# Kernel optimization log

Measured on AMD Instinct MI355X. Metric: run time of the kernel, lower is better.

## Reference

```python
import jax, jax.numpy as jnp
import numpy as np

V = 50000      # vocab_size
E = 512        # embed_size
H = 512        # hidden_size
B = 128        # batch
S = 256        # encoder seq len
MAX_OOVS = 12


def setup_inputs() -> dict:
    key = jax.random.key(0)
    ks = jax.random.split(key, 18)
    s = 0.05
    embed_table = jax.random.normal(ks[4], (V, E), jnp.float32) * s
    embed_table = embed_table.at[0].set(0.0)  # padding_idx=0
    return {
        'input_idx':   jax.random.randint(ks[0], (B,), 0, V),
        'encoded':     jax.random.normal(ks[1], (B, S, H), jnp.float32),
        'encoded_idx': jax.random.randint(ks[2], (B, S), 0, V),
        'prev_state':  jax.random.normal(ks[3], (B, H), jnp.float32),
        'weighted':    jnp.zeros((B, 1, H), jnp.float32),
        'embed_table': embed_table,
        'Ws_w':    jax.random.normal(ks[5], (H, H), jnp.float32) * s,
        'Ws_b':    jnp.zeros((H,), jnp.float32),
        'gru_Wih': jax.random.normal(ks[6], (3 * H, E + H), jnp.float32) * s,
        'gru_Whh': jax.random.normal(ks[7], (3 * H, H), jnp.float32) * s,
        'gru_bih': jnp.zeros((3 * H,), jnp.float32),
        'gru_bhh': jnp.zeros((3 * H,), jnp.float32),
        'attn_W':  jax.random.normal(ks[8], (H, 2 * H), jnp.float32) * s,
        'attn_b':  jnp.zeros((H,), jnp.float32),
        'attn_v':  jax.random.normal(ks[9], (H,), jnp.float32) * s,
        'Wo_w':    jax.random.normal(ks[10], (V, 2 * H), jnp.float32) * s,
        'Wo_b':    jnp.zeros((V,), jnp.float32),
        'Wc_w':    jax.random.normal(ks[11], (2 * H, H), jnp.float32) * s,
        'Wc_b':    jnp.zeros((2 * H,), jnp.float32),
    }


def copy_decoder_fwd(input_idx, encoded, encoded_idx, prev_state, weighted,
                     embed_table, Ws_w, Ws_b, gru_Wih, gru_Whh, gru_bih, gru_bhh,
                     attn_W, attn_b, attn_v, Wo_w, Wo_b, Wc_w, Wc_b):
    b, seq, hidden = encoded.shape
    vocab = Wo_w.shape[0]
    dt = encoded.dtype

    # order == 0 branch: project prev_state, zero the weighted context
    prev = prev_state @ Ws_w.T + Ws_b                      # (b, h)
    wtd = jnp.zeros((b, hidden), dt)                       # (b, h)

    # GRU single step (PyTorch gate layout: r, z, n)
    x = jnp.concatenate([embed_table[input_idx], wtd], axis=1)  # (b, e+h)
    gi = x @ gru_Wih.T + gru_bih                           # (b, 3h)
    gh = prev @ gru_Whh.T + gru_bhh                        # (b, 3h)
    i_r, i_z, i_n = jnp.split(gi, 3, axis=1)
    h_r, h_z, h_n = jnp.split(gh, 3, axis=1)
    r = jax.nn.sigmoid(i_r + h_r)
    z = jax.nn.sigmoid(i_z + h_z)
    n = jnp.tanh(i_n + r * h_n)
    state = (1.0 - z) * n + z * prev                       # (b, h), == rnn_output

    # 'concat' attention: softmax_seq(v . tanh(W[h; enc] + b))
    h_exp = jnp.broadcast_to(state[:, None, :], (b, seq, hidden))
    energy = jnp.tanh(jnp.concatenate([h_exp, encoded], axis=-1) @ attn_W.T + attn_b)
    attn_w = jax.nn.softmax(energy @ attn_v, axis=1)       # (b, seq)
    context = jnp.einsum('bs,bsh->bh', attn_w, encoded)    # (b, h)

    # generation scores
    score_g = jnp.concatenate([state, context], axis=1) @ Wo_w.T + Wo_b  # (b, V)

    # copy scores
    sc = jnp.tanh(encoded @ Wc_w.T + Wc_b)                 # (b, seq, 2h)
    score_c = jnp.einsum('bsk,bk->bs', sc, jnp.concatenate([state, context], axis=1))
    score_c = score_c + jnp.where(encoded_idx == 0, -1000.0, 0.0).astype(dt)

    # joint softmax over vocab + seq
    probs = jax.nn.softmax(jnp.concatenate([score_g, score_c], axis=1), axis=1)
    prob_g = probs[:, :vocab]                              # (b, V)
    prob_c = probs[:, vocab:]                              # (b, seq)
    prob_c_given = prob_c / jnp.sum(prob_c)                # global-scalar normalization (faithful)

    # pad generation probs with small oov mass
    vext = vocab + MAX_OOVS
    prob_g_ext = jnp.concatenate(
        [prob_g, jnp.full((b, MAX_OOVS), 1e-4, dt)], axis=1)  # (b, V+oov)

    # copy -> vocab scatter-add (replaces dense one-hot + bmm)
    batch_ids = jnp.broadcast_to(jnp.arange(b)[:, None], (b, seq))
    prob_c_to_g = jnp.zeros((b, vext), dt).at[batch_ids, encoded_idx].add(prob_c)

    out = (prob_g_ext + prob_c_to_g)[:, None, :]           # (b, 1, V+oov)

    # positions in source equal to the current input token
    ind = (encoded_idx == input_idx[:, None]).astype(dt)   # (b, seq)
    ssum = ind.sum(axis=1, keepdims=True)
    ind = jnp.where(ssum > 1.0, ind / ssum, ind)
    attn2 = prob_c_given * ind                             # (b, seq)
    weighted_new = jnp.einsum('bs,bsh->bh', attn2, encoded)[:, None, :]  # (b, 1, h)

    return out, state, weighted_new


def reference(input_idx, encoded, encoded_idx, prev_state, weighted,
              embed_table, Ws_w, Ws_b, gru_Wih, gru_Whh, gru_bih, gru_bhh,
              attn_W, attn_b, attn_v, Wo_w, Wo_b, Wc_w, Wc_b):
    return copy_decoder_fwd(input_idx, encoded, encoded_idx, prev_state, weighted,
                            embed_table, Ws_w, Ws_b, gru_Wih, gru_Whh, gru_bih, gru_bhh,
                            attn_W, attn_b, attn_v, Wo_w, Wo_b, Wc_w, Wc_b)
```

## Files before the change

### kernel.cpp

```cpp
#include <hip/hip_runtime.h>
#include <hip/hip_bf16.h>
#include <math.h>

#define BB 128
#define SS 256
#define HH 512
#define VV 50000
#define VEXT 50012
#define NBLK 782
#define PST 784

typedef __bf16 bf16x8 __attribute__((ext_vector_type(8)));
typedef float f32x4 __attribute__((ext_vector_type(4)));

__device__ __forceinline__ float fast_tanh(float x) {
  float e = __expf(2.0f * x);
  return 1.0f - 2.0f / (e + 1.0f);
}
__device__ __forceinline__ float fast_sigmoid(float x) {
  return 1.0f / (1.0f + __expf(-x));
}
__device__ __forceinline__ bf16x8 cvt8(const float* p) {
  float4 a = *(const float4*)p;
  float4 b = *(const float4*)(p + 4);
  bf16x8 r;
  r[0] = (__bf16)a.x; r[1] = (__bf16)a.y; r[2] = (__bf16)a.z; r[3] = (__bf16)a.w;
  r[4] = (__bf16)b.x; r[5] = (__bf16)b.y; r[6] = (__bf16)b.z; r[7] = (__bf16)b.w;
  return r;
}

__global__ void k_pack_all(const float* __restrict__ Wc_w, const float* __restrict__ attn_W,
                           const float* __restrict__ enc,
                           __hip_bfloat16* __restrict__ wc_bf,
                           __hip_bfloat16* __restrict__ wa_bf,
                           __hip_bfloat16* __restrict__ epk,
                           float* __restrict__ pc_total) {
  int i = blockIdx.x * 256 + threadIdx.x;
  if (blockIdx.x == 0 && threadIdx.x == 0) pc_total[0] = 0.f;
  if (i < 65536) {
    int l = i & 63, ks = (i >> 6) & 15, tile = i >> 10;
    int m = l & 15, q = l >> 4;
    const float* p = Wc_w + (size_t)(tile * 16 + m) * 512 + ks * 32 + q * 8;
    *(bf16x8*)(wc_bf + (size_t)i * 8) = cvt8(p);
  } else if (i < 98304) {
    int j = i - 65536;
    int l = j & 63, ks = (j >> 6) & 15, tile = j >> 10;
    int m = l & 15, q = l >> 4;
    const float* p = attn_W + (size_t)(tile * 16 + m) * 1024 + 512 + ks * 32 + q * 8;
    *(bf16x8*)(wa_bf + (size_t)j * 8) = cvt8(p);
  } else if (i < 98304 + 2097152) {
    int j = i - 98304;
    int l = j & 63, ks = (j >> 6) & 15, st = (j >> 10) & 15, b = j >> 14;
    int m = l & 15, q = l >> 4;
    const float* p = enc + ((size_t)b * SS + st * 16 + m) * HH + ks * 32 + q * 8;
    *(bf16x8*)(epk + (size_t)j * 8) = cvt8(p);
  }
}

__global__ void k_pack_y(const float* __restrict__ y, __hip_bfloat16* __restrict__ ypk) {
  int i = blockIdx.x * 256 + threadIdx.x;
  int l = i & 63, ks = (i >> 6) & 31, tile = i >> 11;
  int m = l & 15, q = l >> 4;
  const float* p = y + (size_t)(tile * 16 + m) * 1024 + ks * 32 + q * 8;
  *(bf16x8*)(ypk + (size_t)i * 8) = cvt8(p);
}

template <int LDB, bool GATHER>
__global__ __launch_bounds__(256, 2) void k_gemm_bt(
    const float* __restrict__ A, const float* __restrict__ B,
    const float* __restrict__ bias, float* __restrict__ C, int ldc,
    const int* __restrict__ gidx) {
  __shared__ __hip_bfloat16 ylds[128 * 72];
  const int t = threadIdx.x;
  const int l = t & 63, w = t >> 6;
  const int m = l & 15, q = l >> 4;
  const int n = blockIdx.x * 64 + w * 16 + m;
  const float* wrow = B + (size_t)n * LDB;
  f32x4 acc[8];
#pragma unroll
  for (int mt = 0; mt < 8; ++mt) acc[mt] = (f32x4){0.f, 0.f, 0.f, 0.f};

  for (int kt = 0; kt < 512; kt += 64) {
    __syncthreads();
#pragma unroll
    for (int i = 0; i < 8; ++i) {
      int f = t + i * 256;
      int row = f >> 4, c4 = f & 15;
      const float* arow;
      if (GATHER)
        arow = A + (size_t)gidx[row] * 512;
      else
        arow = A + (size_t)row * 512;
      float4 v = *(const float4*)(arow + kt + c4 * 4);
      __hip_bfloat16* d = ylds + row * 72 + c4 * 4;
      d[0] = __float2bfloat16(v.x); d[1] = __float2bfloat16(v.y);
      d[2] = __float2bfloat16(v.z); d[3] = __float2bfloat16(v.w);
    }
    __syncthreads();
#pragma unroll
    for (int ksl = 0; ksl < 2; ++ksl) {
      bf16x8 bfr = cvt8(wrow + kt + ksl * 32 + q * 8);
#pragma unroll
      for (int mt = 0; mt < 8; ++mt) {
        bf16x8 af = *(const bf16x8*)(ylds + (mt * 16 + m) * 72 + ksl * 32 + q * 8);
        acc[mt] = __builtin_amdgcn_mfma_f32_16x16x32_bf16(af, bfr, acc[mt], 0, 0, 0);
      }
    }
  }
  float bv = bias[n];
#pragma unroll
  for (int mt = 0; mt < 8; ++mt) {
#pragma unroll
    for (int r = 0; r < 4; ++r) {
      int rowm = mt * 16 + q * 4 + r;
      C[(size_t)rowm * ldc + n] = acc[mt][r] + bv;
    }
  }
}

__global__ void k_gates(const float* __restrict__ gi, const float* __restrict__ gh,
                        const float* __restrict__ prevv, float* __restrict__ state,
                        float* __restrict__ state_out) {
  int i = blockIdx.x * 256 + threadIdx.x;
  int b = i >> 9, h = i & 511;
  const float* gib = gi + (size_t)b * 1536;
  const float* ghb = gh + (size_t)b * 1536;
  float ir = gib[h], iz = gib[512 + h], inn = gib[1024 + h];
  float hr = ghb[h], hz = ghb[512 + h], hn = ghb[1024 + h];
  float r = fast_sigmoid(ir + hr);
  float z = fast_sigmoid(iz + hz);
  float n = fast_tanh(inn + r * hn);
  float st = (1.f - z) * n + z * prevv[i];
  state[i] = st;
  state_out[i] = st;
}

template <int NTOT, int MODE>
__global__ __launch_bounds__(256, 3) void k_fused(
    const __hip_bfloat16* __restrict__ epack, const __hip_bfloat16* __restrict__ wpk,
    const float* __restrict__ biasA, const float* __restrict__ multA,
    const int* __restrict__ enc_idx, float* __restrict__ out) {
  const int b = blockIdx.x, s0 = blockIdx.y * 32, t = threadIdx.x;
  const int l = t & 63, w = t >> 6;
  const int wm = w & 1, wn = w >> 1;
  const int m = l & 15, q = l >> 4;
  __shared__ float bias_l[NTOT];
  __shared__ float mult_l[NTOT];
  __shared__ float red[2][32];
  const float* bias_base = (MODE == 0) ? biasA + (size_t)b * HH : biasA;
  const float* mult_base = (MODE == 0) ? multA : multA + (size_t)b * 1024;
  for (int i = t; i < NTOT; i += 256) {
    bias_l[i] = bias_base[i];
    mult_l[i] = mult_base[i];
  }
  const int st = blockIdx.y * 2 + wm;
  const __hip_bfloat16* ep = epack + ((size_t)(b * 16 + st) * 16) * 512 + (size_t)l * 8;
  bf16x8 afr[16];
#pragma unroll
  for (int ks = 0; ks < 16; ++ks) afr[ks] = *(const bf16x8*)(ep + ks * 512);
  __syncthreads();

  float part[4] = {0.f, 0.f, 0.f, 0.f};
  for (int nb = 0; nb < NTOT; nb += 32) {
    const __hip_bfloat16* wp = wpk + ((size_t)((nb >> 4) + wn) * 16) * 512 + (size_t)l * 8;
    bf16x8 bfr[16];
#pragma unroll
    for (int ks = 0; ks < 16; ++ks) bfr[ks] = *(const bf16x8*)(wp + ks * 512);
    f32x4 a0 = {0.f, 0.f, 0.f, 0.f}, a1 = a0, a2 = a0, a3 = a0;
#pragma unroll
    for (int j = 0; j < 4; ++j) {
      a0 = __builtin_amdgcn_mfma_f32_16x16x32_bf16(afr[j], bfr[j], a0, 0, 0, 0);
      a1 = __builtin_amdgcn_mfma_f32_16x16x32_bf16(afr[4 + j], bfr[4 + j], a1, 0, 0, 0);
      a2 = __builtin_amdgcn_mfma_f32_16x16x32_bf16(afr[8 + j], bfr[8 + j], a2, 0, 0, 0);
      a3 = __builtin_amdgcn_mfma_f32_16x16x32_bf16(afr[12 + j], bfr[12 + j], a3, 0, 0, 0);
    }
    f32x4 acc = (a0 + a1) + (a2 + a3);
    const int n = nb + wn * 16 + m;
    float bias = bias_l[n];
    float mul = mult_l[n];
#pragma unroll
    for (int r = 0; r < 4; ++r) part[r] += fast_tanh(acc[r] + bias) * mul;
  }
#pragma unroll
  for (int r = 0; r < 4; ++r) {
    part[r] += __shfl_xor(part[r], 1, 64);
    part[r] += __shfl_xor(part[r], 2, 64);
    part[r] += __shfl_xor(part[r], 4, 64);
    part[r] += __shfl_xor(part[r], 8, 64);
  }
  if (m == 0) {
#pragma unroll
    for (int r = 0; r < 4; ++r) red[wn][wm * 16 + q * 4 + r] = part[r];
  }
  __syncthreads();
  if (t < 32) {
    float v = red[0][t] + red[1][t];
    int s = s0 + t;
    if (MODE == 1 && enc_idx[b * SS + s] == 0) v -= 1000.0f;
    out[b * SS + s] = v;
  }
}

__global__ __launch_bounds__(256, 4) void k_score_g2(
    const __hip_bfloat16* __restrict__ ypk, const float* __restrict__ Wo_w,
    const float* __restrict__ Wo_b, float* __restrict__ sg,
    float* __restrict__ ppmax, float* __restrict__ ppsum) {
  const int t = threadIdx.x;
  const int l = t & 63, w = t >> 6;
  const int m = l & 15, q = l >> 4;
  const int blk = blockIdx.x;
  const int n = blk * 64 + w * 16 + m;
  const int n_ld = (n < VV) ? n : (VV - 1);
  const float* wrow = Wo_w + (size_t)n_ld * 1024;
  f32x4 acc[8];
#pragma unroll
  for (int mt = 0; mt < 8; ++mt) acc[mt] = (f32x4){0.f, 0.f, 0.f, 0.f};

  for (int ks = 0; ks < 32; ++ks) {
    bf16x8 bfr = cvt8(wrow + ks * 32 + q * 8);
#pragma unroll
    for (int mt = 0; mt < 8; ++mt) {
      bf16x8 af = *(const bf16x8*)(ypk + (((size_t)mt * 32 + ks) * 64 + l) * 8);
      acc[mt] = __builtin_amdgcn_mfma_f32_16x16x32_bf16(af, bfr, acc[mt], 0, 0, 0);
    }
  }

  float bv = (n < VV) ? Wo_b[n] : 0.f;
#pragma unroll
  for (int mt = 0; mt < 8; ++mt) {
#pragma unroll
    for (int r = 0; r < 4; ++r) {
      float v = acc[mt][r] + bv;
      if (n < VV)
        sg[(size_t)(mt * 16 + q * 4 + r) * VV + n] = v;
      else
        v = -1e30f;
      acc[mt][r] = v;
    }
  }

  __shared__ float redA[4][128];
  __shared__ float MS[128];
#pragma unroll
  for (int mt = 0; mt < 8; ++mt) {
#pragma unroll
    for (int r = 0; r < 4; ++r) {
      float mx = acc[mt][r];
      mx = fmaxf(mx, __shfl_xor(mx, 1, 64));
      mx = fmaxf(mx, __shfl_xor(mx, 2, 64));
      mx = fmaxf(mx, __shfl_xor(mx, 4, 64));
      mx = fmaxf(mx, __shfl_xor(mx, 8, 64));
      if (m == 0) redA[w][mt * 16 + q * 4 + r] = mx;
    }
  }
  __syncthreads();
  if (t < 128)
    MS[t] = fmaxf(fmaxf(redA[0][t], redA[1][t]), fmaxf(redA[2][t], redA[3][t]));
  __syncthreads();
#pragma unroll
  for (int mt = 0; mt < 8; ++mt) {
#pragma unroll
    for (int r = 0; r < 4; ++r) {
      float s = __expf(acc[mt][r] - MS[mt * 16 + q * 4 + r]);
      s += __shfl_xor(s, 1, 64);
      s += __shfl_xor(s, 2, 64);
      s += __shfl_xor(s, 4, 64);
      s += __shfl_xor(s, 8, 64);
      if (m == 0) redA[w][mt * 16 + q * 4 + r] = s;
    }
  }
  __syncthreads();
  if (t < 128) {
    ppmax[(size_t)t * PST + blk] = MS[t];
    ppsum[(size_t)t * PST + blk] = redA[0][t] + redA[1][t] + redA[2][t] + redA[3][t];
  }
}

__global__ void k_rowstat_merge(const float* __restrict__ ppmax, const float* __restrict__ ppsum,
                                const float* __restrict__ sc,
                                float* __restrict__ rmax, float* __restrict__ rsum) {
  const int row = blockIdx.x, t = threadIdx.x;
  __shared__ float rb[8];
  __shared__ float MS[1];
  float mrow = sc[row * SS + t];
  for (int i = t; i < NBLK; i += 256) mrow = fmaxf(mrow, ppmax[(size_t)row * PST + i]);
  for (int off = 32; off > 0; off >>= 1) mrow = fmaxf(mrow, __shfl_xor(mrow, off, 64));
  if ((t & 63) == 0) rb[t >> 6] = mrow;
  __syncthreads();
  if (t == 0) MS[0] = fmaxf(fmaxf(rb[0], rb[1]), fmaxf(rb[2], rb[3]));
  __syncthreads();
  float M = MS[0];
  float s = __expf(sc[row * SS + t] - M);
  for (int i = t; i < NBLK; i += 256)
    s += ppsum[(size_t)row * PST + i] * __expf(ppmax[(size_t)row * PST + i] - M);
  for (int off = 32; off > 0; off >>= 1) s += __shfl_xor(s, off, 64);
  if ((t & 63) == 0) rb[4 + (t >> 6)] = s;
  __syncthreads();
  if (t == 0) {
    rmax[row] = M;
    rsum[row] = rb[4] + rb[5] + rb[6] + rb[7];
  }
}

__global__ void k_attn_softmax(const float* __restrict__ score, float* __restrict__ aw) {
  const int b = blockIdx.x, t = threadIdx.x;
  __shared__ float rbuf[8];
  __shared__ float MS[2];
  float x = score[b * SS + t];
  float m = x;
  for (int off = 32; off > 0; off >>= 1) m = fmaxf(m, __shfl_xor(m, off, 64));
  if ((t & 63) == 0) rbuf[t >> 6] = m;
  __syncthreads();
  if (t == 0) MS[0] = fmaxf(fmaxf(rbuf[0], rbuf[1]), fmaxf(rbuf[2], rbuf[3]));
  __syncthreads();
  float e = __expf(x - MS[0]);
  float s = e;
  for (int off = 32; off > 0; off >>= 1) s += __shfl_xor(s, off, 64);
  if ((t & 63) == 0) rbuf[4 + (t >> 6)] = s;
  __syncthreads();
  if (t == 0) MS[1] = rbuf[4] + rbuf[5] + rbuf[6] + rbuf[7];
  __syncthreads();
  aw[b * SS + t] = e / MS[1];
}

__global__ void k_context(const float* __restrict__ aw, const float* __restrict__ enc,
                          const float* __restrict__ state, float* __restrict__ y) {
  const int b = blockIdx.x, hc = blockIdx.y, t = threadIdx.x;
  __shared__ float aws[SS];
  aws[t] = aw[b * SS + t];
  aws[t + 128] = aw[b * SS + t + 128];
  __syncthreads();
  int h = hc * 128 + t;
  float acc = 0.f;
  for (int s = 0; s < SS; ++s) acc += aws[s] * enc[((size_t)b * SS + s) * HH + h];
  y[(size_t)b * 1024 + HH + h] = acc;
  y[(size_t)b * 1024 + h] = state[b * HH + h];
}

__global__ void k_write_probg(const float* __restrict__ sg,
                              const float* __restrict__ rmax,
                              const float* __restrict__ rsum,
                              float* __restrict__ out) {
  int i = blockIdx.x * 256 + threadIdx.x;
  const int total = BB * VEXT;
  if (i >= total) return;
  int b = i / VEXT;
  int v = i - b * VEXT;
  float val;
  if (v < VV)
    val = __expf(sg[(size_t)b * VV + v] - rmax[b]) / rsum[b];
  else
    val = 1e-4f;
  out[i] = val;
}

__global__ void k_probc(const float* __restrict__ sc,
                        const int* __restrict__ enc_idx,
                        const float* __restrict__ rmax,
                        const float* __restrict__ rsum,
                        float* __restrict__ prob_c,
                        float* __restrict__ out,
                        float* __restrict__ pc_total) {
  const int b = blockIdx.x, t = threadIdx.x;
  __shared__ float rbuf[8];
  float pc = __expf(sc[b * SS + t] - rmax[b]) / rsum[b];
  prob_c[b * SS + t] = pc;
  atomicAdd(&out[(size_t)b * VEXT + enc_idx[b * SS + t]], pc);
  float s = pc;
  for (int off = 32; off > 0; off >>= 1) s += __shfl_down(s, off, 64);
  if ((t & 63) == 0) rbuf[t >> 6] = s;
  __syncthreads();
  if (t == 0) atomicAdd(pc_total, rbuf[0] + rbuf[1] + rbuf[2] + rbuf[3]);
}

__global__ void k_weighted(const int* __restrict__ enc_idx,
                           const int* __restrict__ input_idx,
                           const float* __restrict__ prob_c,
                           const float* __restrict__ pc_total,
                           const float* __restrict__ enc,
                           float* __restrict__ wout) {
  const int b = blockIdx.x, hc = blockIdx.y, t = threadIdx.x;
  __shared__ float f[SS];
  __shared__ float rb[2];
  const int idx_in = input_idx[b];
  int m0 = (enc_idx[b * SS + t] == idx_in) ? 1 : 0;
  int m1 = (enc_idx[b * SS + t + 128] == idx_in) ? 1 : 0;
  float lsum = (float)(m0 + m1);
  for (int off = 32; off > 0; off >>= 1) lsum += __shfl_xor(lsum, off, 64);
  if ((t & 63) == 0) rb[t >> 6] = lsum;
  __syncthreads();
  float tot = rb[0] + rb[1];
  float norm = (tot > 1.0f) ? 1.0f / tot : 1.0f;
  float inv_pct = 1.0f / pc_total[0];
  f[t] = m0 ? prob_c[b * SS + t] * inv_pct * norm : 0.f;
  f[t + 128] = m1 ? prob_c[b * SS + t + 128] * inv_pct * norm : 0.f;
  __syncthreads();
  int h = hc * 128 + t;
  float acc = 0.f;
  for (int s = 0; s < SS; ++s) acc += f[s] * enc[((size_t)b * SS + s) * HH + h];
  wout[b * HH + h] = acc;
}

extern "C" void kernel_launch(void* const* d_in, const int* in_sizes, int n_in,
                              void* d_out, int out_size, void* d_ws, size_t ws_size,
                              hipStream_t stream) {
  const int* input_idx = (const int*)d_in[0];
  const float* encoded = (const float*)d_in[1];
  const int* encoded_idx = (const int*)d_in[2];
  const float* prev_state = (const float*)d_in[3];
  const float* embed = (const float*)d_in[5];
  const float* Ws_w = (const float*)d_in[6];
  const float* Ws_b = (const float*)d_in[7];
  const float* gWih = (const float*)d_in[8];
  const float* gWhh = (const float*)d_in[9];
  const float* gbih = (const float*)d_in[10];
  const float* gbhh = (const float*)d_in[11];
  const float* attn_W = (const float*)d_in[12];
  const float* attn_b = (const float*)d_in[13];
  const float* attn_v = (const float*)d_in[14];
  const float* Wo_w = (const float*)d_in[15];
  const float* Wo_b = (const float*)d_in[16];
  const float* Wc_w = (const float*)d_in[17];
  const float* Wc_b = (const float*)d_in[18];

  float* out = (float*)d_out;
  float* out_state = out + (size_t)BB * VEXT;
  float* out_weighted = out_state + BB * HH;

  float* ws = (float*)d_ws;
  float* prevv = ws;
  float* state = prevv + BB * HH;
  float* hW = state + BB * HH;
  float* ascore = hW + BB * HH;
  float* aw = ascore + BB * SS;
  float* y = aw + BB * SS;
  float* sg = y + BB * 1024;
  float* sc = sg + (size_t)BB * VV;
  float* prob_c = sc + BB * SS;
  float* rmax = prob_c + BB * SS;
  float* rsum = rmax + BB;
  float* pc_total = rsum + BB;
  float* ppmax = pc_total + 64;
  float* ppsum = ppmax + (size_t)BB * PST;
  __hip_bfloat16* wc_bf = (__hip_bfloat16*)(ppsum + (size_t)BB * PST);
  __hip_bfloat16* wa_bf = wc_bf + (size_t)1024 * HH;
  __hip_bfloat16* epack = wa_bf + (size_t)512 * HH;
  __hip_bfloat16* ypk = epack + (size_t)BB * SS * HH;

  float* gi = sg;
  float* gh = sg + BB * 1536;

  k_pack_all<<<8576, 256, 0, stream>>>(Wc_w, attn_W, encoded, wc_bf, wa_bf, epack, pc_total);

  k_gemm_bt<512, false><<<8, 256, 0, stream>>>(prev_state, Ws_w, Ws_b, prevv, 512, nullptr);
  k_gemm_bt<1024, true><<<24, 256, 0, stream>>>(embed, gWih, gbih, gi, 1536, input_idx);
  k_gemm_bt<512, false><<<24, 256, 0, stream>>>(prevv, gWhh, gbhh, gh, 1536, nullptr);
  k_gates<<<256, 256, 0, stream>>>(gi, gh, prevv, state, out_state);
  k_gemm_bt<1024, false><<<8, 256, 0, stream>>>(state, attn_W, attn_b, hW, 512, nullptr);

  k_fused<HH, 0><<<dim3(BB, 8), 256, 0, stream>>>(epack, wa_bf, hW, attn_v,
                                                  nullptr, ascore);
  k_attn_softmax<<<BB, 256, 0, stream>>>(ascore, aw);
  k_context<<<dim3(BB, 4), 128, 0, stream>>>(aw, encoded, state, y);
  k_pack_y<<<64, 256, 0, stream>>>(y, ypk);

  k_score_g2<<<NBLK, 256, 0, stream>>>(ypk, Wo_w, Wo_b, sg, ppmax, ppsum);
  k_fused<1024, 1><<<dim3(BB, 8), 256, 0, stream>>>(epack, wc_bf, Wc_b, y,
                                                    encoded_idx, sc);

  k_rowstat_merge<<<BB, 256, 0, stream>>>(ppmax, ppsum, sc, rmax, rsum);
  k_write_probg<<<(BB * VEXT + 255) / 256, 256, 0, stream>>>(sg, rmax, rsum, out);
  k_probc<<<BB, 256, 0, stream>>>(sc, encoded_idx, rmax, rsum, prob_c, out, pc_total);
  k_weighted<<<dim3(BB, 4), 128, 0, stream>>>(encoded_idx, input_idx, prob_c, pc_total,
                                              encoded, out_weighted);
}
```

Measured before the change: 718.0 us.

## Fuse small kernels and stage attention weights through LDS in fused scorer

Merges the two independent small GEMMs (Ws projection and gathered input GRU GEMM) into one dual-dispatch launch. The attention softmax, context and y-packing are folded into one kernel that writes the packed bf16 y directly. Prob_c computation is folded into the rowstat merge, and the copy scatter-add into the weighted kernel. The fused attention/copy scorer now gives each wave its own 16-row tile and stages weight tiles in LDS shared by all four waves, replacing the cross-wave reduction. The aim is fewer launches and less redundant global weight traffic, at the cost of more LDS per block and lower occupancy (launch bounds 3 to 2).

```diff
diff --git a/kernel.cpp b/kernel.cpp
--- a/kernel.cpp
+++ b/kernel.cpp
@@ -57,14 +57,6 @@
   }
 }
 
-__global__ void k_pack_y(const float* __restrict__ y, __hip_bfloat16* __restrict__ ypk) {
-  int i = blockIdx.x * 256 + threadIdx.x;
-  int l = i & 63, ks = (i >> 6) & 31, tile = i >> 11;
-  int m = l & 15, q = l >> 4;
-  const float* p = y + (size_t)(tile * 16 + m) * 1024 + ks * 32 + q * 8;
-  *(bf16x8*)(ypk + (size_t)i * 8) = cvt8(p);
-}
-
 template <int LDB, bool GATHER>
 __global__ __launch_bounds__(256, 2) void k_gemm_bt(
     const float* __restrict__ A, const float* __restrict__ B,
@@ -91,6 +83,63 @@
         arow = A + (size_t)gidx[row] * 512;
       else
         arow = A + (size_t)row * 512;
+      float4 v = *(const float4*)(arow + kt + c4 * 4);
+      __hip_bfloat16* d = ylds + row * 72 + c4 * 4;
+      d[0] = __float2bfloat16(v.x); d[1] = __float2bfloat16(v.y);
+      d[2] = __float2bfloat16(v.z); d[3] = __float2bfloat16(v.w);
+    }
+    __syncthreads();
+#pragma unroll
+    for (int ksl = 0; ksl < 2; ++ksl) {
+      bf16x8 bfr = cvt8(wrow + kt + ksl * 32 + q * 8);
+#pragma unroll
+      for (int mt = 0; mt < 8; ++mt) {
+        bf16x8 af = *(const bf16x8*)(ylds + (mt * 16 + m) * 72 + ksl * 32 + q * 8);
+        acc[mt] = __builtin_amdgcn_mfma_f32_16x16x32_bf16(af, bfr, acc[mt], 0, 0, 0);
+      }
+    }
+  }
+  float bv = bias[n];
+#pragma unroll
+  for (int mt = 0; mt < 8; ++mt) {
+#pragma unroll
+    for (int r = 0; r < 4; ++r) {
+      int rowm = mt * 16 + q * 4 + r;
+      C[(size_t)rowm * ldc + n] = acc[mt][r] + bv;
+    }
+  }
+}
+
+__global__ __launch_bounds__(256, 2) void k_gemm_dual(
+    const float* __restrict__ A0, const float* __restrict__ B0,
+    const float* __restrict__ b0, float* __restrict__ C0, int ldb0, int ldc0, int nb0,
+    const float* __restrict__ A1, const float* __restrict__ B1,
+    const float* __restrict__ b1, float* __restrict__ C1, int ldb1, int ldc1,
+    const int* __restrict__ gidx1) {
+  __shared__ __hip_bfloat16 ylds[128 * 72];
+  const float* A; const float* Bw; const float* bias; float* C;
+  int ldb, ldc, blk; const int* gidx;
+  if ((int)blockIdx.x < nb0) {
+    A = A0; Bw = B0; bias = b0; C = C0; ldb = ldb0; ldc = ldc0; gidx = nullptr; blk = blockIdx.x;
+  } else {
+    A = A1; Bw = B1; bias = b1; C = C1; ldb = ldb1; ldc = ldc1; gidx = gidx1; blk = blockIdx.x - nb0;
+  }
+  const int t = threadIdx.x;
+  const int l = t & 63, w = t >> 6;
+  const int m = l & 15, q = l >> 4;
+  const int n = blk * 64 + w * 16 + m;
+  const float* wrow = Bw + (size_t)n * ldb;
+  f32x4 acc[8];
+#pragma unroll
+  for (int mt = 0; mt < 8; ++mt) acc[mt] = (f32x4){0.f, 0.f, 0.f, 0.f};
+
+  for (int kt = 0; kt < 512; kt += 64) {
+    __syncthreads();
+#pragma unroll
+    for (int i = 0; i < 8; ++i) {
+      int f = t + i * 256;
+      int row = f >> 4, c4 = f & 15;
+      const float* arow = gidx ? (A + (size_t)gidx[row] * 512) : (A + (size_t)row * 512);
       float4 v = *(const float4*)(arow + kt + c4 * 4);
       __hip_bfloat16* d = ylds + row * 72 + c4 * 4;
       d[0] = __float2bfloat16(v.x); d[1] = __float2bfloat16(v.y);
@@ -136,50 +185,54 @@
 }
 
 template <int NTOT, int MODE>
-__global__ __launch_bounds__(256, 3) void k_fused(
+__global__ __launch_bounds__(256, 2) void k_fused2(
     const __hip_bfloat16* __restrict__ epack, const __hip_bfloat16* __restrict__ wpk,
     const float* __restrict__ biasA, const float* __restrict__ multA,
     const int* __restrict__ enc_idx, float* __restrict__ out) {
-  const int b = blockIdx.x, s0 = blockIdx.y * 32, t = threadIdx.x;
+  const int b = blockIdx.x, t = threadIdx.x;
   const int l = t & 63, w = t >> 6;
-  const int wm = w & 1, wn = w >> 1;
   const int m = l & 15, q = l >> 4;
+  const int st = blockIdx.y * 4 + w;
+  __shared__ __hip_bfloat16 wstage[32 * 512];
   __shared__ float bias_l[NTOT];
   __shared__ float mult_l[NTOT];
-  __shared__ float red[2][32];
   const float* bias_base = (MODE == 0) ? biasA + (size_t)b * HH : biasA;
   const float* mult_base = (MODE == 0) ? multA : multA + (size_t)b * 1024;
   for (int i = t; i < NTOT; i += 256) {
     bias_l[i] = bias_base[i];
     mult_l[i] = mult_base[i];
   }
-  const int st = blockIdx.y * 2 + wm;
   const __hip_bfloat16* ep = epack + ((size_t)(b * 16 + st) * 16) * 512 + (size_t)l * 8;
   bf16x8 afr[16];
 #pragma unroll
   for (int ks = 0; ks < 16; ++ks) afr[ks] = *(const bf16x8*)(ep + ks * 512);
-  __syncthreads();
 
   float part[4] = {0.f, 0.f, 0.f, 0.f};
   for (int nb = 0; nb < NTOT; nb += 32) {
-    const __hip_bfloat16* wp = wpk + ((size_t)((nb >> 4) + wn) * 16) * 512 + (size_t)l * 8;
-    bf16x8 bfr[16];
-#pragma unroll
-    for (int ks = 0; ks < 16; ++ks) bfr[ks] = *(const bf16x8*)(wp + ks * 512);
-    f32x4 a0 = {0.f, 0.f, 0.f, 0.f}, a1 = a0, a2 = a0, a3 = a0;
-#pragma unroll
-    for (int j = 0; j < 4; ++j) {
-      a0 = __builtin_amdgcn_mfma_f32_16x16x32_bf16(afr[j], bfr[j], a0, 0, 0, 0);
-      a1 = __builtin_amdgcn_mfma_f32_16x16x32_bf16(afr[4 + j], bfr[4 + j], a1, 0, 0, 0);
-      a2 = __builtin_amdgcn_mfma_f32_16x16x32_bf16(afr[8 + j], bfr[8 + j], a2, 0, 0, 0);
-      a3 = __builtin_amdgcn_mfma_f32_16x16x32_bf16(afr[12 + j], bfr[12 + j], a3, 0, 0, 0);
-    }
-    f32x4 acc = (a0 + a1) + (a2 + a3);
-    const int n = nb + wn * 16 + m;
-    float bias = bias_l[n];
-    float mul = mult_l[n];
-#pragma unroll
-    for (int r = 0; r < 4; ++r) part[r] += fast_tanh(acc[r] + bias) * mul;
+    __syncthreads();
+    const bf16x8* src = (const bf16x8*)(wpk + (size_t)nb * 512);
+    bf16x8* dstv = (bf16x8*)wstage;
+#pragma unroll
+    for (int i = 0; i < 8; ++i) dstv[t + i * 256] = src[t + i * 256];
+    __syncthreads();
+#pragma unroll
+    for (int nt = 0; nt < 2; ++nt) {
+      const __hip_bfloat16* wbase = wstage + nt * 8192 + (size_t)l * 8;
+      f32x4 a0 = {0.f, 0.f, 0.f, 0.f}, a1 = a0, a2 = a0, a3 = a0;
+#pragma unroll
+      for (int j = 0; j < 4; ++j) {
+        a0 = __builtin_amdgcn_mfma_f32_16x16x32_bf16(afr[j], *(const bf16x8*)(wbase + j * 512), a0, 0, 0, 0);
+        a1 = __builtin_amdgcn_mfma_f32_16x16x32_bf16(afr[4 + j], *(const bf16x8*)(wbase + (4 + j) * 512), a1, 0, 0, 0);
+        a2 = __builtin_amdgcn_mfma_f32_16x16x32_bf16(afr[8 + j], *(const bf16x8*)(wbase + (8 + j) * 512), a2, 0, 0, 0);
+        a3 = __builtin_amdgcn_mfma_f32_16x16x32_bf16(afr[12 + j], *(const bf16x8*)(wbase + (12 + j) * 512), a3, 0, 0, 0);
+      }
+      f32x4 acc = (a0 + a1) + (a2 + a3);
+      const int n = nb + nt * 16 + m;
+      float bias = bias_l[n];
+      float mul = mult_l[n];
+#pragma unroll
+      for (int r = 0; r < 4; ++r) part[r] += fast_tanh(acc[r] + bias) * mul;
+    }
   }
 #pragma unroll
   for (int r = 0; r < 4; ++r) {
@@ -190,14 +243,12 @@
   }
   if (m == 0) {
 #pragma unroll
-    for (int r = 0; r < 4; ++r) red[wn][wm * 16 + q * 4 + r] = part[r];
-  }
-  __syncthreads();
-  if (t < 32) {
-    float v = red[0][t] + red[1][t];
-    int s = s0 + t;
-    if (MODE == 1 && enc_idx[b * SS + s] == 0) v -= 1000.0f;
-    out[b * SS + s] = v;
+    for (int r = 0; r < 4; ++r) {
+      int s = st * 16 + q * 4 + r;
+      float v = part[r];
+      if (MODE == 1 && enc_idx[b * SS + s] == 0) v -= 1000.0f;
+      out[b * SS + s] = v;
+    }
   }
 }
 
@@ -276,13 +327,15 @@
   }
 }
 
-__global__ void k_rowstat_merge(const float* __restrict__ ppmax, const float* __restrict__ ppsum,
-                                const float* __restrict__ sc,
-                                float* __restrict__ rmax, float* __restrict__ rsum) {
+__global__ void k_merge(const float* __restrict__ ppmax, const float* __restrict__ ppsum,
+                        const float* __restrict__ sc,
+                        float* __restrict__ rmax, float* __restrict__ rsum,
+                        float* __restrict__ prob_c, float* __restrict__ pc_total) {
   const int row = blockIdx.x, t = threadIdx.x;
   __shared__ float rb[8];
-  __shared__ float MS[1];
-  float mrow = sc[row * SS + t];
+  __shared__ float MS[2];
+  float x_sc = sc[row * SS + t];
+  float mrow = x_sc;
   for (int i = t; i < NBLK; i += 256) mrow = fmaxf(mrow, ppmax[(size_t)row * PST + i]);
   for (int off = 32; off > 0; off >>= 1) mrow = fmaxf(mrow, __shfl_xor(mrow, off, 64));
   if ((t & 63) == 0) rb[t >> 6] = mrow;
@@ -290,51 +343,63 @@
   if (t == 0) MS[0] = fmaxf(fmaxf(rb[0], rb[1]), fmaxf(rb[2], rb[3]));
   __syncthreads();
   float M = MS[0];
-  float s = __expf(sc[row * SS + t] - M);
+  float e_sc = __expf(x_sc - M);
+  float s = e_sc;
   for (int i = t; i < NBLK; i += 256)
     s += ppsum[(size_t)row * PST + i] * __expf(ppmax[(size_t)row * PST + i] - M);
   for (int off = 32; off > 0; off >>= 1) s += __shfl_xor(s, off, 64);
   if ((t & 63) == 0) rb[4 + (t >> 6)] = s;
   __syncthreads();
+  if (t == 0) MS[1] = rb[4] + rb[5] + rb[6] + rb[7];
+  __syncthreads();
+  float S = MS[1];
   if (t == 0) {
     rmax[row] = M;
-    rsum[row] = rb[4] + rb[5] + rb[6] + rb[7];
-  }
-}
-
-__global__ void k_attn_softmax(const float* __restrict__ score, float* __restrict__ aw) {
-  const int b = blockIdx.x, t = threadIdx.x;
-  __shared__ float rbuf[8];
-  __shared__ float MS[2];
-  float x = score[b * SS + t];
-  float m = x;
-  for (int off = 32; off > 0; off >>= 1) m = fmaxf(m, __shfl_xor(m, off, 64));
-  if ((t & 63) == 0) rbuf[t >> 6] = m;
-  __syncthreads();
-  if (t == 0) MS[0] = fmaxf(fmaxf(rbuf[0], rbuf[1]), fmaxf(rbuf[2], rbuf[3]));
-  __syncthreads();
-  float e = __expf(x - MS[0]);
-  float s = e;
-  for (int off = 32; off > 0; off >>= 1) s += __shfl_xor(s, off, 64);
-  if ((t & 63) == 0) rbuf[4 + (t >> 6)] = s;
-  __syncthreads();
-  if (t == 0) MS[1] = rbuf[4] + rbuf[5] + rbuf[6] + rbuf[7];
-  __syncthreads();
-  aw[b * SS + t] = e / MS[1];
-}
-
-__global__ void k_context(const float* __restrict__ aw, const float* __restrict__ enc,
-                          const float* __restrict__ state, float* __restrict__ y) {
+    rsum[row] = S;
+  }
+  float pc = e_sc / S;
+  prob_c[row * SS + t] = pc;
+  float ps = pc;
+  for (int off = 32; off > 0; off >>= 1) ps += __shfl_xor(ps, off, 64);
+  if ((t & 63) == 0) rb[t >> 6] = ps;
+  __syncthreads();
+  if (t == 0) atomicAdd(pc_total, rb[0] + rb[1] + rb[2] + rb[3]);
+}
+
+__global__ void k_ctx(const float* __restrict__ score, const float* __restrict__ enc,
+                      const float* __restrict__ state, float* __restrict__ y,
+                      __hip_bfloat16* __restrict__ ypk) {
   const int b = blockIdx.x, hc = blockIdx.y, t = threadIdx.x;
   __shared__ float aws[SS];
-  aws[t] = aw[b * SS + t];
-  aws[t + 128] = aw[b * SS + t + 128];
-  __syncthreads();
-  int h = hc * 128 + t;
+  __shared__ float rb[4];
+  float x0 = score[b * SS + t], x1 = score[b * SS + t + 128];
+  float mx = fmaxf(x0, x1);
+  for (int off = 32; off > 0; off >>= 1) mx = fmaxf(mx, __shfl_xor(mx, off, 64));
+  if ((t & 63) == 0) rb[t >> 6] = mx;
+  __syncthreads();
+  mx = fmaxf(rb[0], rb[1]);
+  float e0 = __expf(x0 - mx), e1 = __expf(x1 - mx);
+  float s = e0 + e1;
+  for (int off = 32; off > 0; off >>= 1) s += __shfl_xor(s, off, 64);
+  if ((t & 63) == 0) rb[2 + (t >> 6)] = s;
+  __syncthreads();
+  float inv = 1.0f / (rb[2] + rb[3]);
+  aws[t] = e0 * inv;
+  aws[t + 128] = e1 * inv;
+  __syncthreads();
+  const int h = hc * 128 + t;
   float acc = 0.f;
-  for (int s = 0; s < SS; ++s) acc += aws[s] * enc[((size_t)b * SS + s) * HH + h];
+#pragma unroll 8
+  for (int ss = 0; ss < SS; ++ss) acc += aws[ss] * enc[((size_t)b * SS + ss) * HH + h];
+  float sv = state[b * HH + h];
+  y[(size_t)b * 1024 + h] = sv;
   y[(size_t)b * 1024 + HH + h] = acc;
-  y[(size_t)b * 1024 + h] = state[b * HH + h];
+  const int tile = b >> 4, mm = b & 15;
+  const int c0 = h, c1 = HH + h;
+  ypk[(((size_t)tile * 32 + (c0 >> 5)) * 64 + ((c0 & 31) >> 3) * 16 + mm) * 8 + (c0 & 7)] =
+      __float2bfloat16(sv);
+  ypk[(((size_t)tile * 32 + (c1 >> 5)) * 64 + ((c1 & 31) >> 3) * 16 + mm) * 8 + (c1 & 7)] =
+      __float2bfloat16(acc);
 }
 
 __global__ void k_write_probg(const float* __restrict__ sg,
@@ -354,37 +419,25 @@
   out[i] = val;
 }
 
-__global__ void k_probc(const float* __restrict__ sc,
-                        const int* __restrict__ enc_idx,
-                        const float* __restrict__ rmax,
-                        const float* __restrict__ rsum,
-                        float* __restrict__ prob_c,
-                        float* __restrict__ out,
-                        float* __restrict__ pc_total) {
-  const int b = blockIdx.x, t = threadIdx.x;
-  __shared__ float rbuf[8];
-  float pc = __expf(sc[b * SS + t] - rmax[b]) / rsum[b];
-  prob_c[b * SS + t] = pc;
-  atomicAdd(&out[(size_t)b * VEXT + enc_idx[b * SS + t]], pc);
-  float s = pc;
-  for (int off = 32; off > 0; off >>= 1) s += __shfl_down(s, off, 64);
-  if ((t & 63) == 0) rbuf[t >> 6] = s;
-  __syncthreads();
-  if (t == 0) atomicAdd(pc_total, rbuf[0] + rbuf[1] + rbuf[2] + rbuf[3]);
-}
-
-__global__ void k_weighted(const int* __restrict__ enc_idx,
-                           const int* __restrict__ input_idx,
-                           const float* __restrict__ prob_c,
-                           const float* __restrict__ pc_total,
-                           const float* __restrict__ enc,
-                           float* __restrict__ wout) {
+__global__ void k_weighted2(const int* __restrict__ enc_idx,
+                            const int* __restrict__ input_idx,
+                            const float* __restrict__ prob_c,
+                            const float* __restrict__ pc_total,
+                            const float* __restrict__ enc,
+                            float* __restrict__ wout,
+                            float* __restrict__ out) {
   const int b = blockIdx.x, hc = blockIdx.y, t = threadIdx.x;
   __shared__ float f[SS];
   __shared__ float rb[2];
   const int idx_in = input_idx[b];
-  int m0 = (enc_idx[b * SS + t] == idx_in) ? 1 : 0;
-  int m1 = (enc_idx[b * SS + t + 128] == idx_in) ? 1 : 0;
+  const int e0i = enc_idx[b * SS + t], e1i = enc_idx[b * SS + t + 128];
+  const float p0 = prob_c[b * SS + t], p1 = prob_c[b * SS + t + 128];
+  if (hc == 0) {
+    atomicAdd(&out[(size_t)b * VEXT + e0i], p0);
+    atomicAdd(&out[(size_t)b * VEXT + e1i], p1);
+  }
+  int m0 = (e0i == idx_in) ? 1 : 0;
+  int m1 = (e1i == idx_in) ? 1 : 0;
   float lsum = (float)(m0 + m1);
   for (int off = 32; off > 0; off >>= 1) lsum += __shfl_xor(lsum, off, 64);
   if ((t & 63) == 0) rb[t >> 6] = lsum;
@@ -392,12 +445,12 @@
   float tot = rb[0] + rb[1];
   float norm = (tot > 1.0f) ? 1.0f / tot : 1.0f;
   float inv_pct = 1.0f / pc_total[0];
-  f[t] = m0 ? prob_c[b * SS + t] * inv_pct * norm : 0.f;
-  f[t + 128] = m1 ? prob_c[b * SS + t + 128] * inv_pct * norm : 0.f;
-  __syncthreads();
-  int h = hc * 128 + t;
+  f[t] = m0 ? p0 * inv_pct * norm : 0.f;
+  f[t + 128] = m1 ? p1 * inv_pct * norm : 0.f;
+  __syncthreads();
+  const int h = hc * 128 + t;
   float acc = 0.f;
-  for (int s = 0; s < SS; ++s) acc += f[s] * enc[((size_t)b * SS + s) * HH + h];
+  for (int ss = 0; ss < SS; ++ss) acc += f[ss] * enc[((size_t)b * SS + ss) * HH + h];
   wout[b * HH + h] = acc;
 }
 
@@ -452,25 +505,22 @@
 
   k_pack_all<<<8576, 256, 0, stream>>>(Wc_w, attn_W, encoded, wc_bf, wa_bf, epack, pc_total);
 
-  k_gemm_bt<512, false><<<8, 256, 0, stream>>>(prev_state, Ws_w, Ws_b, prevv, 512, nullptr);
-  k_gemm_bt<1024, true><<<24, 256, 0, stream>>>(embed, gWih, gbih, gi, 1536, input_idx);
+  k_gemm_dual<<<32, 256, 0, stream>>>(prev_state, Ws_w, Ws_b, prevv, 512, 512, 8,
+                                      embed, gWih, gbih, gi, 1024, 1536, input_idx);
   k_gemm_bt<512, false><<<24, 256, 0, stream>>>(prevv, gWhh, gbhh, gh, 1536, nullptr);
   k_gates<<<256, 256, 0, stream>>>(gi, gh, prevv, state, out_state);
   k_gemm_bt<1024, false><<<8, 256, 0, stream>>>(state, attn_W, attn_b, hW, 512, nullptr);
 
-  k_fused<HH, 0><<<dim3(BB, 8), 256, 0, stream>>>(epack, wa_bf, hW, attn_v,
-                                                  nullptr, ascore);
-  k_attn_softmax<<<BB, 256, 0, stream>>>(ascore, aw);
-  k_context<<<dim3(BB, 4), 128, 0, stream>>>(aw, encoded, state, y);
-  k_pack_y<<<64, 256, 0, stream>>>(y, ypk);
+  k_fused2<HH, 0><<<dim3(BB, 4), 256, 0, stream>>>(epack, wa_bf, hW, attn_v,
+                                                   nullptr, ascore);
+  k_ctx<<<dim3(BB, 4), 128, 0, stream>>>(ascore, encoded, state, y, ypk);
 
   k_score_g2<<<NBLK, 256, 0, stream>>>(ypk, Wo_w, Wo_b, sg, ppmax, ppsum);
-  k_fused<1024, 1><<<dim3(BB, 8), 256, 0, stream>>>(epack, wc_bf, Wc_b, y,
-                                                    encoded_idx, sc);
-
-  k_rowstat_merge<<<BB, 256, 0, stream>>>(ppmax, ppsum, sc, rmax, rsum);
+  k_fused2<1024, 1><<<dim3(BB, 4), 256, 0, stream>>>(epack, wc_bf, Wc_b, y,
+                                                     encoded_idx, sc);
+
+  k_merge<<<BB, 256, 0, stream>>>(ppmax, ppsum, sc, rmax, rsum, prob_c, pc_total);
   k_write_probg<<<(BB * VEXT + 255) / 256, 256, 0, stream>>>(sg, rmax, rsum, out);
-  k_probc<<<BB, 256, 0, stream>>>(sc, encoded_idx, rmax, rsum, prob_c, out, pc_total);
-  k_weighted<<<dim3(BB, 4), 128, 0, stream>>>(encoded_idx, input_idx, prob_c, pc_total,
-                                              encoded, out_weighted);
-}
+  k_weighted2<<<dim3(BB, 4), 128, 0, stream>>>(encoded_idx, input_idx, prob_c, pc_total,
+                                               encoded, out_weighted, out);
+}
```

Result: slower. 808.8 us (+12.6%).
